# Kernel optimization log

Hardware: AMD Instinct MI355X
Metric: run time of the kernel (lower is better)

The kernel has to match this reference:

```python
import jax, jax.numpy as jnp
import numpy as np

EPS = 1e-5  # torch InstanceNorm1d default


def _instance_norm_lastdim(t):
    # torch InstanceNorm1d applied to (b*h, n, d): normalizes over last axis d
    # per (b, h, n) with biased variance, no affine.
    mu = jnp.mean(t, axis=-1, keepdims=True)
    var = jnp.var(t, axis=-1, keepdims=True)
    return (t - mu) * jax.lax.rsqrt(var + EPS)


def setup_inputs() -> dict:
    key = jax.random.key(0)
    k1, k2, k3, k4 = jax.random.split(key, 4)
    b, n, dim = 4, 8192, 128
    heads, dim_head = 8, 64
    inner = heads * dim_head
    x = jax.random.normal(k1, (b, n, dim), dtype=jnp.float32)
    # nn.Linear(dim, inner*3, bias=False): weight (out, in); we store transposed (in, out)
    w_qkv = jax.random.normal(k2, (dim, inner * 3), dtype=jnp.float32) * (1.0 / np.sqrt(dim))
    w_out = jax.random.normal(k3, (inner, dim), dtype=jnp.float32) * (1.0 / np.sqrt(inner))
    b_out = jax.random.normal(k4, (dim,), dtype=jnp.float32) * 0.01
    return {"x": x, "w_qkv": w_qkv, "w_out": w_out, "b_out": b_out}


def reference(x, w_qkv, w_out, b_out):
    b, n, _ = x.shape
    heads, dim_head = 8, 64
    qkv = x @ w_qkv  # (b, n, 3*inner)
    q, k, v = jnp.split(qkv, 3, axis=-1)

    def to_heads(t):
        return t.reshape(b, n, heads, dim_head).transpose(0, 2, 1, 3)  # b h n d

    q, k, v = to_heads(q), to_heads(k), to_heads(v)
    # galerkin: norm k and v (InstanceNorm over dim_head axis)
    k = _instance_norm_lastdim(k)
    v = _instance_norm_lastdim(v)
    dots = jnp.einsum('bhnd,bhne->bhde', k, v)      # K^T V, small (d x d)
    out = jnp.einsum('bhnd,bhde->bhne', q, dots) * (1.0 / n)
    out = out.transpose(0, 2, 1, 3).reshape(b, n, heads * dim_head)
    return out @ w_out + b_out
```

## Files before the change

kernel.cpp:

```cpp
#include <hip/hip_runtime.h>

#define NN 8192
#define DIM 128

typedef short short8 __attribute__((ext_vector_type(8)));
typedef float f32x4 __attribute__((ext_vector_type(4)));

__device__ __forceinline__ unsigned short f2bf(float f) {
  unsigned int u = __float_as_uint(f);
  u = (u + 0x7FFFu + ((u >> 16) & 1u)) >> 16;
  return (unsigned short)u;
}
__device__ __forceinline__ unsigned int cvtpk(float a, float b) {
  unsigned int r;
  asm("v_cvt_pk_bf16_f32 %0, %1, %2" : "=v"(r) : "v"(a), "v"(b));
  return r;
}
__device__ __forceinline__ void gll16(const void* gsrc, void* ldst) {
  __builtin_amdgcn_global_load_lds(
      (const __attribute__((address_space(1))) unsigned int*)gsrc,
      (__attribute__((address_space(3))) unsigned int*)ldst, 16, 0, 0);
}
#define BAR_LGKM()                                          \
  do {                                                      \
    asm volatile("s_waitcnt lgkmcnt(0)" ::: "memory");      \
    __builtin_amdgcn_sched_barrier(0);                      \
    __builtin_amdgcn_s_barrier();                           \
    __builtin_amdgcn_sched_barrier(0);                      \
  } while (0)
#define BAR_VM()                                            \
  do {                                                      \
    asm volatile("s_waitcnt vmcnt(0)" ::: "memory");        \
    __builtin_amdgcn_sched_barrier(0);                      \
    __builtin_amdgcn_s_barrier();                           \
    __builtin_amdgcn_sched_barrier(0);                      \
  } while (0)

__global__ __launch_bounds__(256) void prep_kernel(const float* __restrict__ x,
                                                   const float* __restrict__ wqkv,
                                                   unsigned char* __restrict__ ximg,
                                                   unsigned char* __restrict__ wimg,
                                                   float* __restrict__ dots) {
  __shared__ __align__(16) unsigned char wb[32768];
  const int t = threadIdx.x;
  const int bx = blockIdx.x;
  if (bx < 1024) {
#pragma unroll
    for (int rep = 0; rep < 2; ++rep) {
      const int idx = bx * 512 + rep * 256 + t;
      const int bt = idx >> 10;
      const int o = (idx & 1023) << 4;
      const int r = o >> 8;
      const int q0 = o & 255;
      const int c0 = (q0 ^ ((r & 7) << 4)) >> 1;
      const float* src = x + ((size_t)(bt >> 7) * NN + (size_t)(bt & 127) * 64 + r) * DIM + c0;
      const float4 v0 = *(const float4*)src;
      const float4 v1 = *(const float4*)(src + 4);
      uint4 u;
      u.x = cvtpk(v0.x, v0.y);
      u.y = cvtpk(v0.z, v0.w);
      u.z = cvtpk(v1.x, v1.y);
      u.w = cvtpk(v1.z, v1.w);
      *(uint4*)(ximg + (size_t)idx * 16) = u;
    }
  } else if (bx < 1032) {
    const int h = bx - 1024;
    const int k = t >> 1;
    const int chalf = t & 1;
    const float* wp = wqkv + (size_t)k * 1536 + (chalf ? (1024 + h * 64) : (512 + h * 64));
    const float4* wp4 = (const float4*)wp;
    const int c0 = chalf * 64;
    float4 wv[16];
    float sum = 0.f;
#pragma unroll
    for (int jj = 0; jj < 16; ++jj) {
      wv[jj] = wp4[jj];
      sum += wv[jj].x + wv[jj].y + wv[jj].z + wv[jj].w;
    }
    const float mean = sum * (1.f / 64.f);
#pragma unroll
    for (int jj = 0; jj < 16; ++jj) {
      const int c = c0 + jj * 4;
      const unsigned int cx0 = (unsigned int)((c + 0) & 7) << 4;
      const unsigned int cx1 = (unsigned int)((c + 1) & 7) << 4;
      const unsigned int cx2 = (unsigned int)((c + 2) & 7) << 4;
      const unsigned int cx3 = (unsigned int)((c + 3) & 7) << 4;
      *(unsigned short*)(wb + (c + 0) * 256 + (((unsigned)(2 * k)) ^ cx0)) = f2bf(wv[jj].x - mean);
      *(unsigned short*)(wb + (c + 1) * 256 + (((unsigned)(2 * k)) ^ cx1)) = f2bf(wv[jj].y - mean);
      *(unsigned short*)(wb + (c + 2) * 256 + (((unsigned)(2 * k)) ^ cx2)) = f2bf(wv[jj].z - mean);
      *(unsigned short*)(wb + (c + 3) * 256 + (((unsigned)(2 * k)) ^ cx3)) = f2bf(wv[jj].w - mean);
    }
    __syncthreads();
    const uint4* s4 = (const uint4*)(wb + t * 128);
    uint4* d4 = (uint4*)(wimg + (size_t)h * 32768 + t * 128);
#pragma unroll
    for (int i = 0; i < 8; ++i) d4[i] = s4[i];
  } else {
    const int zb = bx - 1032;
    float4* dz = (float4*)dots + (size_t)zb * 4096 + t;
    const float4 z = make_float4(0.f, 0.f, 0.f, 0.f);
#pragma unroll
    for (int i = 0; i < 16; ++i) dz[i * 256] = z;
  }
}

__global__ __launch_bounds__(256, 4) void kv_dots_v4(const unsigned char* __restrict__ ximg,
                                                     const unsigned char* __restrict__ wimg,
                                                     float* __restrict__ dots) {
  __shared__ __align__(16) unsigned char smem[40960];
  unsigned char* const WB = smem;
  unsigned char* const KT = smem + 32768;
  unsigned char* const VT = smem + 36864;

  const int t = threadIdx.x;
  const int bx = blockIdx.x;
  const int h = bx >> 7;
  const int p = bx & 127;
  const int b = p >> 5;
  const int chunk = p & 31;

  const int wave = t >> 6;
  const int lane = t & 63;
  const int lb = lane & 15;
  const int kg = lane >> 4;
  const int g = wave & 1;
  const int ch = wave >> 1;
  const unsigned int lxor = (unsigned int)(lb & 7) << 4;
  const unsigned int rxor = (unsigned int)(lb & 3) << 4;

  const unsigned char* wsrc = wimg + (size_t)h * 32768;
  const unsigned char* xsrc = ximg + (size_t)(b * 128 + chunk * 4) * 16384;

#pragma unroll
  for (int i = 0; i < 8; ++i)
    gll16(wsrc + (i * 4 + wave) * 1024 + lane * 16, WB + (i * 4 + wave) * 1024);

  const int rrow = 16 * g + lb;
  short8 xf[4];
#pragma unroll
  for (int ks = 0; ks < 4; ++ks)
    xf[ks] = *(const short8*)(xsrc + rrow * 256 + (((unsigned)(ks * 64 + kg * 16)) ^ lxor));

  f32x4 dacc[4];
#pragma unroll
  for (int et = 0; et < 4; ++et) dacc[et] = (f32x4)0.f;

  BAR_VM();

  unsigned char* const MYT = ch ? VT : KT;

  for (int tile = 0; tile < 8; ++tile) {
    short8 xn[4];
    if (tile < 7) {
      const unsigned char* tb = xsrc + (size_t)((tile + 1) >> 1) * 16384 + (size_t)((tile + 1) & 1) * 8192;
#pragma unroll
      for (int ks = 0; ks < 4; ++ks)
        xn[ks] = *(const short8*)(tb + rrow * 256 + (((unsigned)(ks * 64 + kg * 16)) ^ lxor));
    }

    f32x4 acc[4];
#pragma unroll
    for (int ct = 0; ct < 4; ++ct) acc[ct] = (f32x4)0.f;
#pragma unroll
    for (int ks = 0; ks < 4; ++ks) {
      const unsigned int koff = ((unsigned)(ks * 64 + kg * 16)) ^ lxor;
#pragma unroll
      for (int ct = 0; ct < 4; ++ct) {
        const short8 bf = *(const short8*)(WB + (ch * 64 + ct * 16 + lb) * 256 + koff);
        acc[ct] = __builtin_amdgcn_mfma_f32_16x16x32_bf16(xf[ks], bf, acc[ct], 0, 0, 0);
      }
    }

    float sc[4];
#pragma unroll
    for (int e = 0; e < 4; ++e) {
      float s = acc[0][e] * acc[0][e] + acc[1][e] * acc[1][e] +
                acc[2][e] * acc[2][e] + acc[3][e] * acc[3][e];
      s += __shfl_xor(s, 1);
      s += __shfl_xor(s, 2);
      s += __shfl_xor(s, 4);
      s += __shfl_xor(s, 8);
      sc[e] = rsqrtf(s * (1.f / 64.f) + 1e-5f);
    }

    {
      const unsigned int rb = ((unsigned)(g * 32 + kg * 8)) ^ rxor;
#pragma unroll
      for (int ct = 0; ct < 4; ++ct) {
        uint2 w2;
        w2.x = cvtpk(acc[ct][0] * sc[0], acc[ct][1] * sc[1]);
        w2.y = cvtpk(acc[ct][2] * sc[2], acc[ct][3] * sc[3]);
        *(uint2*)(MYT + (ct * 16 + lb) * 64 + rb) = w2;
      }
    }
    BAR_LGKM();

    {
      const unsigned int soff = ((unsigned)(kg * 16)) ^ rxor;
      const short8 a = *(const short8*)(KT + (wave * 16 + lb) * 64 + soff);
#pragma unroll
      for (int et = 0; et < 4; ++et) {
        const short8 bf = *(const short8*)(VT + (et * 16 + lb) * 64 + soff);
        dacc[et] = __builtin_amdgcn_mfma_f32_16x16x32_bf16(a, bf, dacc[et], 0, 0, 0);
      }
    }
    BAR_LGKM();

#pragma unroll
    for (int ks = 0; ks < 4; ++ks) xf[ks] = xn[ks];
  }

  float* dp = dots + (size_t)(b * 8 + h) * 4096;
#pragma unroll
  for (int et = 0; et < 4; ++et) {
#pragma unroll
    for (int reg = 0; reg < 4; ++reg) {
      const int d = wave * 16 + kg * 4 + reg;
      const int e = et * 16 + lb;
      atomicAdd(&dp[d * 64 + e], dacc[et][reg]);
    }
  }
}

template <int TR>
__global__ __launch_bounds__(256) void tw_kernel(const float* __restrict__ wqkv,
                                                 const float* __restrict__ wout,
                                                 const float* __restrict__ dots,
                                                 float* __restrict__ part) {
  __shared__ __align__(16) float ds[64 * 66];
  __shared__ __align__(16) float wqT[64 * 36];
  __shared__ __align__(16) float Ts[32 * 66];
  __shared__ __align__(16) float wos[64 * 132];

  const int blk = blockIdx.x;
  const int bh = blk >> 2;
  const int cq = blk & 3;
  const int h = bh & 7;
  const int t = threadIdx.x;

  for (int i = t; i < 4096; i += 256)
    ds[(i >> 6) * 66 + (i & 63)] = dots[(size_t)bh * 4096 + i];

  for (int i = t; i < 2048; i += 256) {
    const int d = i >> 5;
    const int c = i & 31;
    wqT[d * 36 + c] = wqkv[(size_t)(cq * 32 + c) * 1536 + h * 64 + d];
  }

  for (int i = t; i < 2048; i += 256) {
    const int e = i >> 5;
    const int jj = (i & 31) * 4;
    *(float4*)&wos[e * 132 + jj] = *(const float4*)(wout + (size_t)(h * 64 + e) * 128 + jj);
  }
  __syncthreads();

  {
    const int c = t >> 3;
    const int e0 = (t & 7) * 8;
    float acc[8];
#pragma unroll
    for (int q = 0; q < 8; ++q) acc[q] = 0.f;
    for (int d = 0; d < 64; ++d) {
      const float wq = wqT[d * 36 + c];
      const float4 d0 = *(const float4*)&ds[d * 66 + e0];
      const float4 d1 = *(const float4*)&ds[d * 66 + e0 + 4];
      acc[0] += wq * d0.x; acc[1] += wq * d0.y; acc[2] += wq * d0.z; acc[3] += wq * d0.w;
      acc[4] += wq * d1.x; acc[5] += wq * d1.y; acc[6] += wq * d1.z; acc[7] += wq * d1.w;
    }
    *(float4*)&Ts[c * 66 + e0] = make_float4(acc[0], acc[1], acc[2], acc[3]);
    *(float4*)&Ts[c * 66 + e0 + 4] = make_float4(acc[4], acc[5], acc[6], acc[7]);
  }
  __syncthreads();

  {
    const int c = t >> 3;
    const int j0 = (t & 7) * 16;
    float acc[16];
#pragma unroll
    for (int q = 0; q < 16; ++q) acc[q] = 0.f;
    for (int e = 0; e < 64; ++e) {
      const float tv = Ts[c * 66 + e];
#pragma unroll
      for (int q = 0; q < 16; q += 4) {
        const float4 wv = *(const float4*)&wos[e * 132 + j0 + q];
        acc[q + 0] += tv * wv.x;
        acc[q + 1] += tv * wv.y;
        acc[q + 2] += tv * wv.z;
        acc[q + 3] += tv * wv.w;
      }
    }
    if (TR) {
      float* pp = part + (size_t)bh * 16384;
      const int cc = cq * 32 + c;
#pragma unroll
      for (int q = 0; q < 16; ++q) pp[(j0 + q) * 128 + cc] = acc[q];
    } else {
      float* pp = part + (size_t)bh * 16384 + (size_t)(cq * 32 + c) * 128 + j0;
#pragma unroll
      for (int q = 0; q < 16; q += 4)
        *(float4*)&pp[q] = make_float4(acc[q], acc[q + 1], acc[q + 2], acc[q + 3]);
    }
  }
}

__global__ __launch_bounds__(256) void bigw_reduce_v2(const float* __restrict__ part,
                                                      unsigned char* __restrict__ bigwimg) {
  const int idx = blockIdx.x * 256 + threadIdx.x;
  const int b = idx >> 11;
  const int o = (idx & 2047) << 4;
  const int j = o >> 8;
  const int q0 = o & 255;
  const int c0 = (q0 ^ ((j & 7) << 4)) >> 1;
  float s[8];
#pragma unroll
  for (int i = 0; i < 8; ++i) s[i] = 0.f;
  const float* pb = part + (size_t)b * 8 * 16384 + j * 128 + c0;
#pragma unroll
  for (int hh = 0; hh < 8; ++hh) {
    const float4 p0 = *(const float4*)(pb + hh * 16384);
    const float4 p1 = *(const float4*)(pb + hh * 16384 + 4);
    s[0] += p0.x; s[1] += p0.y; s[2] += p0.z; s[3] += p0.w;
    s[4] += p1.x; s[5] += p1.y; s[6] += p1.z; s[7] += p1.w;
  }
  const float inv_n = 1.f / (float)NN;
  uint4 u;
  u.x = cvtpk(s[0] * inv_n, s[1] * inv_n);
  u.y = cvtpk(s[2] * inv_n, s[3] * inv_n);
  u.z = cvtpk(s[4] * inv_n, s[5] * inv_n);
  u.w = cvtpk(s[6] * inv_n, s[7] * inv_n);
  *(uint4*)(bigwimg + (size_t)idx * 16) = u;
}

__global__ __launch_bounds__(256) void out_v2(const unsigned char* __restrict__ ximg,
                                              const unsigned char* __restrict__ bigwimg,
                                              const float* __restrict__ bout,
                                              float* __restrict__ out) {
  __shared__ __align__(16) unsigned char smem[49152];
  unsigned char* const XB = smem;
  unsigned char* const WJ = smem + 16384;

  const int t = threadIdx.x;
  const int bx = blockIdx.x;
  const int b = bx >> 7;
  const int tile = bx & 127;

  const int wave = t >> 6;
  const int lane = t & 63;
  const int lb = lane & 15;
  const int kg = lane >> 4;
  const unsigned int lxor = (unsigned int)(lb & 7) << 4;

  const unsigned char* wsrc = bigwimg + (size_t)b * 32768;
  const unsigned char* xsrc = ximg + (size_t)(b * 128 + tile) * 16384;

#pragma unroll
  for (int i = 0; i < 8; ++i)
    gll16(wsrc + (wave * 8 + i) * 1024 + lane * 16, WJ + (wave * 8 + i) * 1024);
#pragma unroll
  for (int i = 0; i < 4; ++i)
    gll16(xsrc + (wave * 4 + i) * 1024 + lane * 16, XB + (wave * 4 + i) * 1024);

  float bias[8];
#pragma unroll
  for (int ct = 0; ct < 8; ++ct) bias[ct] = bout[ct * 16 + lb];

  BAR_VM();

  f32x4 acc[8];
#pragma unroll
  for (int ct = 0; ct < 8; ++ct) acc[ct] = (f32x4)0.f;
  const int arow = wave * 16 + lb;
#pragma unroll
  for (int ks = 0; ks < 4; ++ks) {
    const unsigned int koff = (unsigned int)(ks * 64 + kg * 16);
    const short8 a = *(const short8*)(XB + arow * 256 + (koff ^ lxor));
#pragma unroll
    for (int ct = 0; ct < 8; ++ct) {
      const short8 bf = *(const short8*)(WJ + (ct * 16 + lb) * 256 + (koff ^ lxor));
      acc[ct] = __builtin_amdgcn_mfma_f32_16x16x32_bf16(a, bf, acc[ct], 0, 0, 0);
    }
  }

  float* op = out + (size_t)(b * NN + tile * 64 + 16 * wave + kg * 4) * DIM;
#pragma unroll
  for (int ct = 0; ct < 8; ++ct) {
#pragma unroll
    for (int reg = 0; reg < 4; ++reg) {
      op[reg * DIM + ct * 16 + lb] = acc[ct][reg] + bias[ct];
    }
  }
}

__global__ __launch_bounds__(256) void zero_dots_fb(float* __restrict__ dots) {
  float4* dz = (float4*)dots + (size_t)blockIdx.x * 4096 + threadIdx.x;
  const float4 z = make_float4(0.f, 0.f, 0.f, 0.f);
#pragma unroll
  for (int i = 0; i < 16; ++i) dz[i * 256] = z;
}

__global__ __launch_bounds__(256) void kv_dots_fb(const float* __restrict__ x,
                                                  const float* __restrict__ wqkv,
                                                  float* __restrict__ dots) {
  __shared__ __align__(16) unsigned char smem[49152];
  unsigned char* const XB = smem;
  unsigned char* const KT = smem;
  unsigned char* const VT = smem + 8192;
  unsigned char* const WB = smem + 16384;

  const int t = threadIdx.x;
  const int bx = blockIdx.x;
  const int h = bx >> 7;
  const int p = bx & 127;
  const int b = p >> 5;
  const int chunk = p & 31;
  const int row0 = chunk * 256;

  const int wave = t >> 6;
  const int lane = t & 63;
  const int lb = lane & 15;
  const int kg = lane >> 4;
  const unsigned int lxor = (unsigned int)(lb & 7) << 4;

  {
    const int k = t >> 1;
    const int chalf = t & 1;
    const float* wp = wqkv + (size_t)k * 1536 + (chalf ? (1024 + h * 64) : (512 + h * 64));
    const float4* wp4 = (const float4*)wp;
    const int c0 = chalf * 64;
    float4 wv[16];
    float sum = 0.f;
#pragma unroll
    for (int jj = 0; jj < 16; ++jj) {
      wv[jj] = wp4[jj];
      sum += wv[jj].x + wv[jj].y + wv[jj].z + wv[jj].w;
    }
    const float mean = sum * (1.f / 64.f);
#pragma unroll
    for (int jj = 0; jj < 16; ++jj) {
      const int c = c0 + jj * 4;
      const unsigned int cx0 = (unsigned int)((c + 0) & 7) << 4;
      const unsigned int cx1 = (unsigned int)((c + 1) & 7) << 4;
      const unsigned int cx2 = (unsigned int)((c + 2) & 7) << 4;
      const unsigned int cx3 = (unsigned int)((c + 3) & 7) << 4;
      *(unsigned short*)(WB + (c + 0) * 256 + (((unsigned)(2 * k)) ^ cx0)) = f2bf(wv[jj].x - mean);
      *(unsigned short*)(WB + (c + 1) * 256 + (((unsigned)(2 * k)) ^ cx1)) = f2bf(wv[jj].y - mean);
      *(unsigned short*)(WB + (c + 2) * 256 + (((unsigned)(2 * k)) ^ cx2)) = f2bf(wv[jj].z - mean);
      *(unsigned short*)(WB + (c + 3) * 256 + (((unsigned)(2 * k)) ^ cx3)) = f2bf(wv[jj].w - mean);
    }
  }

  f32x4 dacc[4];
#pragma unroll
  for (int nt = 0; nt < 4; ++nt) dacc[nt] = (f32x4)0.f;

  __syncthreads();

  for (int tile = 0; tile < 4; ++tile) {
    const int rowbase = row0 + tile * 64;
    __syncthreads();
    {
      const int r = t >> 2;
      const int cb = (t & 3) * 32;
      const float4* gp4 = (const float4*)(x + (size_t)(b * NN + rowbase + r) * DIM + cb);
      const unsigned int rxor = (unsigned int)(r & 7) << 4;
#pragma unroll
      for (int jj = 0; jj < 4; ++jj) {
        const float4 v0 = gp4[2 * jj];
        const float4 v1 = gp4[2 * jj + 1];
        uint4 u;
        u.x = cvtpk(v0.x, v0.y);
        u.y = cvtpk(v0.z, v0.w);
        u.z = cvtpk(v1.x, v1.y);
        u.w = cvtpk(v1.z, v1.w);
        *(uint4*)(XB + r * 256 + (((unsigned)(2 * cb + 16 * jj)) ^ rxor)) = u;
      }
    }
    __syncthreads();

    f32x4 acc[8];
#pragma unroll
    for (int ct = 0; ct < 8; ++ct) acc[ct] = (f32x4)0.f;
    const int arow = wave * 16 + lb;
#pragma unroll
    for (int ks = 0; ks < 4; ++ks) {
      const unsigned int koff = (unsigned int)(ks * 64 + kg * 16);
      const short8 a = *(const short8*)(XB + arow * 256 + (koff ^ lxor));
#pragma unroll
      for (int ct = 0; ct < 8; ++ct) {
        const short8 bf = *(const short8*)(WB + (ct * 16 + lb) * 256 + (koff ^ lxor));
        acc[ct] = __builtin_amdgcn_mfma_f32_16x16x32_bf16(a, bf, acc[ct], 0, 0, 0);
      }
    }

    float kscale[4];
#pragma unroll
    for (int e = 0; e < 4; ++e) {
      float sk = acc[0][e] * acc[0][e] + acc[1][e] * acc[1][e] +
                 acc[2][e] * acc[2][e] + acc[3][e] * acc[3][e];
      float sv = acc[4][e] * acc[4][e] + acc[5][e] * acc[5][e] +
                 acc[6][e] * acc[6][e] + acc[7][e] * acc[7][e];
      sk += __shfl_xor(sk, 1); sv += __shfl_xor(sv, 1);
      sk += __shfl_xor(sk, 2); sv += __shfl_xor(sv, 2);
      sk += __shfl_xor(sk, 4); sv += __shfl_xor(sv, 4);
      sk += __shfl_xor(sk, 8); sv += __shfl_xor(sv, 8);
      kscale[e] = rsqrtf(sk * (1.f / 64.f) + 1e-5f) * rsqrtf(sv * (1.f / 64.f) + 1e-5f);
    }

    __syncthreads();
    {
      const unsigned int rb2 = (unsigned int)(32 * wave + kg * 8);
#pragma unroll
      for (int ct = 0; ct < 4; ++ct) {
        uint2 w;
        w.x = cvtpk(acc[ct][0] * kscale[0], acc[ct][1] * kscale[1]);
        w.y = cvtpk(acc[ct][2] * kscale[2], acc[ct][3] * kscale[3]);
        *(uint2*)(KT + (ct * 16 + lb) * 128 + (rb2 ^ lxor)) = w;
      }
#pragma unroll
      for (int ct = 4; ct < 8; ++ct) {
        uint2 w;
        w.x = cvtpk(acc[ct][0], acc[ct][1]);
        w.y = cvtpk(acc[ct][2], acc[ct][3]);
        *(uint2*)(VT + ((ct - 4) * 16 + lb) * 128 + (rb2 ^ lxor)) = w;
      }
    }
    __syncthreads();

#pragma unroll
    for (int ks2 = 0; ks2 < 2; ++ks2) {
      const unsigned int koff = (unsigned int)(ks2 * 64 + kg * 16);
      const short8 a = *(const short8*)(KT + (wave * 16 + lb) * 128 + (koff ^ lxor));
#pragma unroll
      for (int nt = 0; nt < 4; ++nt) {
        const short8 bf = *(const short8*)(VT + (nt * 16 + lb) * 128 + (koff ^ lxor));
        dacc[nt] = __builtin_amdgcn_mfma_f32_16x16x32_bf16(a, bf, dacc[nt], 0, 0, 0);
      }
    }
  }

  float* dp = dots + (size_t)(b * 8 + h) * 4096;
#pragma unroll
  for (int nt = 0; nt < 4; ++nt) {
#pragma unroll
    for (int reg = 0; reg < 4; ++reg) {
      const int d = 16 * wave + kg * 4 + reg;
      const int e = nt * 16 + lb;
      atomicAdd(&dp[d * 64 + e], dacc[nt][reg]);
    }
  }
}

__global__ __launch_bounds__(256) void bigw_reduce_fb(const float* __restrict__ part,
                                                      float* __restrict__ bigw) {
  const int i = blockIdx.x * 256 + threadIdx.x;
  const int b = i >> 14;
  const int cj = i & 16383;
  const float* pp = part + (size_t)b * 8 * 16384 + cj;
  float s = 0.f;
#pragma unroll
  for (int h = 0; h < 8; ++h) s += pp[h * 16384];
  bigw[i] = s * (1.f / (float)NN);
}

__global__ __launch_bounds__(256) void out_fb(const float* __restrict__ x,
                                              const float* __restrict__ bigw,
                                              const float* __restrict__ bout,
                                              float* __restrict__ out) {
  __shared__ __align__(16) unsigned char smem[49152];
  unsigned char* const XB = smem;
  unsigned char* const WB = smem + 16384;

  const int t = threadIdx.x;
  const int bx = blockIdx.x;
  const int b = bx >> 7;
  const int rowbase = (bx & 127) * 64;

  const int wave = t >> 6;
  const int lane = t & 63;
  const int lb = lane & 15;
  const int kg = lane >> 4;
  const unsigned int lxor = (unsigned int)(lb & 7) << 4;

  {
    const int c = t >> 1;
    const int jhalf = t & 1;
    const float4* wp4 = (const float4*)(bigw + (size_t)b * 16384 + (size_t)c * 128 + jhalf * 64);
    const int j0 = jhalf * 64;
#pragma unroll
    for (int q = 0; q < 16; ++q) {
      const float4 v = wp4[q];
      const int j = j0 + q * 4;
      const unsigned int jx0 = (unsigned int)((j + 0) & 7) << 4;
      const unsigned int jx1 = (unsigned int)((j + 1) & 7) << 4;
      const unsigned int jx2 = (unsigned int)((j + 2) & 7) << 4;
      const unsigned int jx3 = (unsigned int)((j + 3) & 7) << 4;
      *(unsigned short*)(WB + (j + 0) * 256 + (((unsigned)(2 * c)) ^ jx0)) = f2bf(v.x);
      *(unsigned short*)(WB + (j + 1) * 256 + (((unsigned)(2 * c)) ^ jx1)) = f2bf(v.y);
      *(unsigned short*)(WB + (j + 2) * 256 + (((unsigned)(2 * c)) ^ jx2)) = f2bf(v.z);
      *(unsigned short*)(WB + (j + 3) * 256 + (((unsigned)(2 * c)) ^ jx3)) = f2bf(v.w);
    }
  }

  float bias[8];
#pragma unroll
  for (int ct = 0; ct < 8; ++ct) bias[ct] = bout[ct * 16 + lb];

  {
    const int r = t >> 2;
    const int cb = (t & 3) * 32;
    const float4* gp4 = (const float4*)(x + (size_t)(b * NN + rowbase + r) * DIM + cb);
    const unsigned int rxor = (unsigned int)(r & 7) << 4;
#pragma unroll
    for (int jj = 0; jj < 4; ++jj) {
      const float4 v0 = gp4[2 * jj];
      const float4 v1 = gp4[2 * jj + 1];
      uint4 u;
      u.x = cvtpk(v0.x, v0.y);
      u.y = cvtpk(v0.z, v0.w);
      u.z = cvtpk(v1.x, v1.y);
      u.w = cvtpk(v1.z, v1.w);
      *(uint4*)(XB + r * 256 + (((unsigned)(2 * cb + 16 * jj)) ^ rxor)) = u;
    }
  }
  __syncthreads();

  f32x4 acc[8];
#pragma unroll
  for (int ct = 0; ct < 8; ++ct) acc[ct] = (f32x4)0.f;
  const int arow = wave * 16 + lb;
#pragma unroll
  for (int ks = 0; ks < 4; ++ks) {
    const unsigned int koff = (unsigned int)(ks * 64 + kg * 16);
    const short8 a = *(const short8*)(XB + arow * 256 + (koff ^ lxor));
#pragma unroll
    for (int ct = 0; ct < 8; ++ct) {
      const short8 bf = *(const short8*)(WB + (ct * 16 + lb) * 256 + (koff ^ lxor));
      acc[ct] = __builtin_amdgcn_mfma_f32_16x16x32_bf16(a, bf, acc[ct], 0, 0, 0);
    }
  }

  float* op = out + (size_t)(b * NN + rowbase + 16 * wave + kg * 4) * DIM;
#pragma unroll
  for (int ct = 0; ct < 8; ++ct) {
#pragma unroll
    for (int reg = 0; reg < 4; ++reg) {
      op[reg * DIM + ct * 16 + lb] = acc[ct][reg] + bias[ct];
    }
  }
}

extern "C" void kernel_launch(void* const* d_in, const int* in_sizes, int n_in,
                              void* d_out, int out_size, void* d_ws, size_t ws_size,
                              hipStream_t stream) {
  (void)in_sizes; (void)n_in; (void)out_size;
  const float* x = (const float*)d_in[0];
  const float* wqkv = (const float*)d_in[1];
  const float* wout = (const float*)d_in[2];
  const float* bout = (const float*)d_in[3];
  float* out = (float*)d_out;

  const size_t NEED = 8388608ull + 262144ull + 131072ull + 524288ull + 2097152ull;
  if (ws_size >= NEED) {
    unsigned char* ximg = (unsigned char*)d_ws;
    unsigned char* wimg = ximg + 8388608;
    unsigned char* bigwimg = wimg + 262144;
    float* dots = (float*)(bigwimg + 131072);
    float* part = dots + 131072;

    hipLaunchKernelGGL(prep_kernel, dim3(1040), dim3(256), 0, stream, x, wqkv, ximg, wimg, dots);
    hipLaunchKernelGGL(kv_dots_v4, dim3(1024), dim3(256), 0, stream, ximg, wimg, dots);
    hipLaunchKernelGGL((tw_kernel<1>), dim3(128), dim3(256), 0, stream, wqkv, wout, dots, part);
    hipLaunchKernelGGL(bigw_reduce_v2, dim3(32), dim3(256), 0, stream, part, bigwimg);
    hipLaunchKernelGGL(out_v2, dim3(512), dim3(256), 0, stream, ximg, bigwimg, bout, out);
  } else {
    float* dots = (float*)d_ws;
    float* part = dots + 131072;
    float* bigw = part + 524288;
    hipLaunchKernelGGL(zero_dots_fb, dim3(8), dim3(256), 0, stream, dots);
    hipLaunchKernelGGL(kv_dots_fb, dim3(1024), dim3(256), 0, stream, x, wqkv, dots);
    hipLaunchKernelGGL((tw_kernel<0>), dim3(128), dim3(256), 0, stream, wqkv, wout, dots, part);
    hipLaunchKernelGGL(bigw_reduce_fb, dim3(256), dim3(256), 0, stream, part, bigw);
    hipLaunchKernelGGL(out_fb, dim3(512), dim3(256), 0, stream, x, bigw, bout, out);
  }
}
```

Measured before the change: 65.87 us.

## Fuse bigw reduction into tw via atomics and double-buffer kv_dots LDS

```diff
diff --git a/kernel.cpp b/kernel.cpp
--- a/kernel.cpp
+++ b/kernel.cpp
@@ -35,12 +35,20 @@
     __builtin_amdgcn_s_barrier();                           \
     __builtin_amdgcn_sched_barrier(0);                      \
   } while (0)
+#define BAR_BOTH()                                                  \
+  do {                                                              \
+    asm volatile("s_waitcnt vmcnt(0) lgkmcnt(0)" ::: "memory");     \
+    __builtin_amdgcn_sched_barrier(0);                              \
+    __builtin_amdgcn_s_barrier();                                   \
+    __builtin_amdgcn_sched_barrier(0);                              \
+  } while (0)
 
 __global__ __launch_bounds__(256) void prep_kernel(const float* __restrict__ x,
                                                    const float* __restrict__ wqkv,
                                                    unsigned char* __restrict__ ximg,
                                                    unsigned char* __restrict__ wimg,
-                                                   float* __restrict__ dots) {
+                                                   float* __restrict__ dots,
+                                                   float* __restrict__ bigw) {
   __shared__ __align__(16) unsigned char wb[32768];
   const int t = threadIdx.x;
   const int bx = blockIdx.x;
@@ -95,22 +103,26 @@
     uint4* d4 = (uint4*)(wimg + (size_t)h * 32768 + t * 128);
 #pragma unroll
     for (int i = 0; i < 8; ++i) d4[i] = s4[i];
-  } else {
+  } else if (bx < 1040) {
     const int zb = bx - 1032;
     float4* dz = (float4*)dots + (size_t)zb * 4096 + t;
     const float4 z = make_float4(0.f, 0.f, 0.f, 0.f);
 #pragma unroll
     for (int i = 0; i < 16; ++i) dz[i * 256] = z;
-  }
-}
-
-__global__ __launch_bounds__(256, 4) void kv_dots_v4(const unsigned char* __restrict__ ximg,
+  } else {
+    const int zb = bx - 1040;
+    float4* bz = (float4*)bigw + (size_t)zb * 4096 + t;
+    const float4 z = make_float4(0.f, 0.f, 0.f, 0.f);
+#pragma unroll
+    for (int i = 0; i < 16; ++i) bz[i * 256] = z;
+  }
+}
+
+__global__ __launch_bounds__(256, 3) void kv_dots_v5(const unsigned char* __restrict__ ximg,
                                                      const unsigned char* __restrict__ wimg,
                                                      float* __restrict__ dots) {
-  __shared__ __align__(16) unsigned char smem[40960];
+  __shared__ __align__(16) unsigned char smem[49152];
   unsigned char* const WB = smem;
-  unsigned char* const KT = smem + 32768;
-  unsigned char* const VT = smem + 36864;
 
   const int t = threadIdx.x;
   const int bx = blockIdx.x;
@@ -147,8 +159,6 @@
 
   BAR_VM();
 
-  unsigned char* const MYT = ch ? VT : KT;
-
   for (int tile = 0; tile < 8; ++tile) {
     short8 xn[4];
     if (tile < 7) {
@@ -183,7 +193,9 @@
       sc[e] = rsqrtf(s * (1.f / 64.f) + 1e-5f);
     }
 
+    unsigned char* const BUF = smem + 32768 + (tile & 1) * 8192;
     {
+      unsigned char* const MYT = BUF + ch * 4096;
       const unsigned int rb = ((unsigned)(g * 32 + kg * 8)) ^ rxor;
 #pragma unroll
       for (int ct = 0; ct < 4; ++ct) {
@@ -197,14 +209,13 @@
 
     {
       const unsigned int soff = ((unsigned)(kg * 16)) ^ rxor;
-      const short8 a = *(const short8*)(KT + (wave * 16 + lb) * 64 + soff);
+      const short8 a = *(const short8*)(BUF + (wave * 16 + lb) * 64 + soff);
 #pragma unroll
       for (int et = 0; et < 4; ++et) {
-        const short8 bf = *(const short8*)(VT + (et * 16 + lb) * 64 + soff);
+        const short8 bf = *(const short8*)(BUF + 4096 + (et * 16 + lb) * 64 + soff);
         dacc[et] = __builtin_amdgcn_mfma_f32_16x16x32_bf16(a, bf, dacc[et], 0, 0, 0);
       }
     }
-    BAR_LGKM();
 
 #pragma unroll
     for (int ks = 0; ks < 4; ++ks) xf[ks] = xn[ks];
@@ -222,11 +233,10 @@
   }
 }
 
-template <int TR>
-__global__ __launch_bounds__(256) void tw_kernel(const float* __restrict__ wqkv,
-                                                 const float* __restrict__ wout,
-                                                 const float* __restrict__ dots,
-                                                 float* __restrict__ part) {
+__global__ __launch_bounds__(256) void tw_v3(const float* __restrict__ wqkv,
+                                             const float* __restrict__ wout,
+                                             const float* __restrict__ dots,
+                                             float* __restrict__ bigw) {
   __shared__ __align__(16) float ds[64 * 66];
   __shared__ __align__(16) float wqT[64 * 36];
   __shared__ __align__(16) float Ts[32 * 66];
@@ -289,50 +299,15 @@
         acc[q + 3] += tv * wv.w;
       }
     }
-    if (TR) {
-      float* pp = part + (size_t)bh * 16384;
-      const int cc = cq * 32 + c;
-#pragma unroll
-      for (int q = 0; q < 16; ++q) pp[(j0 + q) * 128 + cc] = acc[q];
-    } else {
-      float* pp = part + (size_t)bh * 16384 + (size_t)(cq * 32 + c) * 128 + j0;
-#pragma unroll
-      for (int q = 0; q < 16; q += 4)
-        *(float4*)&pp[q] = make_float4(acc[q], acc[q + 1], acc[q + 2], acc[q + 3]);
-    }
-  }
-}
-
-__global__ __launch_bounds__(256) void bigw_reduce_v2(const float* __restrict__ part,
-                                                      unsigned char* __restrict__ bigwimg) {
-  const int idx = blockIdx.x * 256 + threadIdx.x;
-  const int b = idx >> 11;
-  const int o = (idx & 2047) << 4;
-  const int j = o >> 8;
-  const int q0 = o & 255;
-  const int c0 = (q0 ^ ((j & 7) << 4)) >> 1;
-  float s[8];
-#pragma unroll
-  for (int i = 0; i < 8; ++i) s[i] = 0.f;
-  const float* pb = part + (size_t)b * 8 * 16384 + j * 128 + c0;
-#pragma unroll
-  for (int hh = 0; hh < 8; ++hh) {
-    const float4 p0 = *(const float4*)(pb + hh * 16384);
-    const float4 p1 = *(const float4*)(pb + hh * 16384 + 4);
-    s[0] += p0.x; s[1] += p0.y; s[2] += p0.z; s[3] += p0.w;
-    s[4] += p1.x; s[5] += p1.y; s[6] += p1.z; s[7] += p1.w;
-  }
-  const float inv_n = 1.f / (float)NN;
-  uint4 u;
-  u.x = cvtpk(s[0] * inv_n, s[1] * inv_n);
-  u.y = cvtpk(s[2] * inv_n, s[3] * inv_n);
-  u.z = cvtpk(s[4] * inv_n, s[5] * inv_n);
-  u.w = cvtpk(s[6] * inv_n, s[7] * inv_n);
-  *(uint4*)(bigwimg + (size_t)idx * 16) = u;
-}
-
-__global__ __launch_bounds__(256) void out_v2(const unsigned char* __restrict__ ximg,
-                                              const unsigned char* __restrict__ bigwimg,
+    const float inv_n = 1.f / (float)NN;
+    float* bp = bigw + (size_t)(bh >> 3) * 16384 + (size_t)(cq * 32 + c) * 128 + j0;
+#pragma unroll
+    for (int q = 0; q < 16; ++q) atomicAdd(&bp[q], acc[q] * inv_n);
+  }
+}
+
+__global__ __launch_bounds__(256) void out_v3(const unsigned char* __restrict__ ximg,
+                                              const float* __restrict__ bigw,
                                               const float* __restrict__ bout,
                                               float* __restrict__ out) {
   __shared__ __align__(16) unsigned char smem[49152];
@@ -350,21 +325,36 @@
   const int kg = lane >> 4;
   const unsigned int lxor = (unsigned int)(lb & 7) << 4;
 
-  const unsigned char* wsrc = bigwimg + (size_t)b * 32768;
   const unsigned char* xsrc = ximg + (size_t)(b * 128 + tile) * 16384;
-
-#pragma unroll
-  for (int i = 0; i < 8; ++i)
-    gll16(wsrc + (wave * 8 + i) * 1024 + lane * 16, WJ + (wave * 8 + i) * 1024);
 #pragma unroll
   for (int i = 0; i < 4; ++i)
     gll16(xsrc + (wave * 4 + i) * 1024 + lane * 16, XB + (wave * 4 + i) * 1024);
 
+  {
+    const int c = t >> 1;
+    const int jhalf = t & 1;
+    const float4* wp4 = (const float4*)(bigw + (size_t)b * 16384 + (size_t)c * 128 + jhalf * 64);
+    const int j0 = jhalf * 64;
+#pragma unroll
+    for (int q = 0; q < 16; ++q) {
+      const float4 v = wp4[q];
+      const int j = j0 + q * 4;
+      const unsigned int jx0 = (unsigned int)((j + 0) & 7) << 4;
+      const unsigned int jx1 = (unsigned int)((j + 1) & 7) << 4;
+      const unsigned int jx2 = (unsigned int)((j + 2) & 7) << 4;
+      const unsigned int jx3 = (unsigned int)((j + 3) & 7) << 4;
+      *(unsigned short*)(WJ + (j + 0) * 256 + (((unsigned)(2 * c)) ^ jx0)) = f2bf(v.x);
+      *(unsigned short*)(WJ + (j + 1) * 256 + (((unsigned)(2 * c)) ^ jx1)) = f2bf(v.y);
+      *(unsigned short*)(WJ + (j + 2) * 256 + (((unsigned)(2 * c)) ^ jx2)) = f2bf(v.z);
+      *(unsigned short*)(WJ + (j + 3) * 256 + (((unsigned)(2 * c)) ^ jx3)) = f2bf(v.w);
+    }
+  }
+
   float bias[8];
 #pragma unroll
   for (int ct = 0; ct < 8; ++ct) bias[ct] = bout[ct * 16 + lb];
 
-  BAR_VM();
+  BAR_BOTH();
 
   f32x4 acc[8];
 #pragma unroll
@@ -547,6 +537,79 @@
       const int e = nt * 16 + lb;
       atomicAdd(&dp[d * 64 + e], dacc[nt][reg]);
     }
+  }
+}
+
+__global__ __launch_bounds__(256) void tw_fb(const float* __restrict__ wqkv,
+                                             const float* __restrict__ wout,
+                                             const float* __restrict__ dots,
+                                             float* __restrict__ part) {
+  __shared__ __align__(16) float ds[64 * 66];
+  __shared__ __align__(16) float wqT[64 * 36];
+  __shared__ __align__(16) float Ts[32 * 66];
+  __shared__ __align__(16) float wos[64 * 132];
+
+  const int blk = blockIdx.x;
+  const int bh = blk >> 2;
+  const int cq = blk & 3;
+  const int h = bh & 7;
+  const int t = threadIdx.x;
+
+  for (int i = t; i < 4096; i += 256)
+    ds[(i >> 6) * 66 + (i & 63)] = dots[(size_t)bh * 4096 + i];
+
+  for (int i = t; i < 2048; i += 256) {
+    const int d = i >> 5;
+    const int c = i & 31;
+    wqT[d * 36 + c] = wqkv[(size_t)(cq * 32 + c) * 1536 + h * 64 + d];
+  }
+
+  for (int i = t; i < 2048; i += 256) {
+    const int e = i >> 5;
+    const int jj = (i & 31) * 4;
+    *(float4*)&wos[e * 132 + jj] = *(const float4*)(wout + (size_t)(h * 64 + e) * 128 + jj);
+  }
+  __syncthreads();
+
+  {
+    const int c = t >> 3;
+    const int e0 = (t & 7) * 8;
+    float acc[8];
+#pragma unroll
+    for (int q = 0; q < 8; ++q) acc[q] = 0.f;
+    for (int d = 0; d < 64; ++d) {
+      const float wq = wqT[d * 36 + c];
+      const float4 d0 = *(const float4*)&ds[d * 66 + e0];
+      const float4 d1 = *(const float4*)&ds[d * 66 + e0 + 4];
+      acc[0] += wq * d0.x; acc[1] += wq * d0.y; acc[2] += wq * d0.z; acc[3] += wq * d0.w;
+      acc[4] += wq * d1.x; acc[5] += wq * d1.y; acc[6] += wq * d1.z; acc[7] += wq * d1.w;
+    }
+    *(float4*)&Ts[c * 66 + e0] = make_float4(acc[0], acc[1], acc[2], acc[3]);
+    *(float4*)&Ts[c * 66 + e0 + 4] = make_float4(acc[4], acc[5], acc[6], acc[7]);
+  }
+  __syncthreads();
+
+  {
+    const int c = t >> 3;
+    const int j0 = (t & 7) * 16;
+    float acc[16];
+#pragma unroll
+    for (int q = 0; q < 16; ++q) acc[q] = 0.f;
+    for (int e = 0; e < 64; ++e) {
+      const float tv = Ts[c * 66 + e];
+#pragma unroll
+      for (int q = 0; q < 16; q += 4) {
+        const float4 wv = *(const float4*)&wos[e * 132 + j0 + q];
+        acc[q + 0] += tv * wv.x;
+        acc[q + 1] += tv * wv.y;
+        acc[q + 2] += tv * wv.z;
+        acc[q + 3] += tv * wv.w;
+      }
+    }
+    float* pp = part + (size_t)bh * 16384 + (size_t)(cq * 32 + c) * 128 + j0;
+#pragma unroll
+    for (int q = 0; q < 16; q += 4)
+      *(float4*)&pp[q] = make_float4(acc[q], acc[q + 1], acc[q + 2], acc[q + 3]);
   }
 }
 
@@ -659,26 +722,24 @@
   const float* bout = (const float*)d_in[3];
   float* out = (float*)d_out;
 
-  const size_t NEED = 8388608ull + 262144ull + 131072ull + 524288ull + 2097152ull;
+  const size_t NEED = 8388608ull + 262144ull + 524288ull + 262144ull;
   if (ws_size >= NEED) {
     unsigned char* ximg = (unsigned char*)d_ws;
     unsigned char* wimg = ximg + 8388608;
-    unsigned char* bigwimg = wimg + 262144;
-    float* dots = (float*)(bigwimg + 131072);
-    float* part = dots + 131072;
-
-    hipLaunchKernelGGL(prep_kernel, dim3(1040), dim3(256), 0, stream, x, wqkv, ximg, wimg, dots);
-    hipLaunchKernelGGL(kv_dots_v4, dim3(1024), dim3(256), 0, stream, ximg, wimg, dots);
-    hipLaunchKernelGGL((tw_kernel<1>), dim3(128), dim3(256), 0, stream, wqkv, wout, dots, part);
-    hipLaunchKernelGGL(bigw_reduce_v2, dim3(32), dim3(256), 0, stream, part, bigwimg);
-    hipLaunchKernelGGL(out_v2, dim3(512), dim3(256), 0, stream, ximg, bigwimg, bout, out);
+    float* dots = (float*)(wimg + 262144);
+    float* bigw = dots + 131072;
+
+    hipLaunchKernelGGL(prep_kernel, dim3(1044), dim3(256), 0, stream, x, wqkv, ximg, wimg, dots, bigw);
+    hipLaunchKernelGGL(kv_dots_v5, dim3(1024), dim3(256), 0, stream, ximg, wimg, dots);
+    hipLaunchKernelGGL(tw_v3, dim3(128), dim3(256), 0, stream, wqkv, wout, dots, bigw);
+    hipLaunchKernelGGL(out_v3, dim3(512), dim3(256), 0, stream, ximg, bigw, bout, out);
   } else {
     float* dots = (float*)d_ws;
     float* part = dots + 131072;
     float* bigw = part + 524288;
     hipLaunchKernelGGL(zero_dots_fb, dim3(8), dim3(256), 0, stream, dots);
     hipLaunchKernelGGL(kv_dots_fb, dim3(1024), dim3(256), 0, stream, x, wqkv, dots);
-    hipLaunchKernelGGL((tw_kernel<0>), dim3(128), dim3(256), 0, stream, wqkv, wout, dots, part);
+    hipLaunchKernelGGL(tw_fb, dim3(128), dim3(256), 0, stream, wqkv, wout, dots, part);
     hipLaunchKernelGGL(bigw_reduce_fb, dim3(256), dim3(256), 0, stream, part, bigw);
     hipLaunchKernelGGL(out_fb, dim3(512), dim3(256), 0, stream, x, bigw, bout, out);
   }
```

Measured after the change: 93.34 us. 1.42x slower.

## Replace atomic dots accumulation with per-block partials reduced in tw_kernel

Applied to the files above, without the earlier changes.

```diff
diff --git a/kernel.cpp b/kernel.cpp
--- a/kernel.cpp
+++ b/kernel.cpp
@@ -39,8 +39,7 @@
 __global__ __launch_bounds__(256) void prep_kernel(const float* __restrict__ x,
                                                    const float* __restrict__ wqkv,
                                                    unsigned char* __restrict__ ximg,
-                                                   unsigned char* __restrict__ wimg,
-                                                   float* __restrict__ dots) {
+                                                   unsigned char* __restrict__ wimg) {
   __shared__ __align__(16) unsigned char wb[32768];
   const int t = threadIdx.x;
   const int bx = blockIdx.x;
@@ -63,7 +62,7 @@
       u.w = cvtpk(v1.z, v1.w);
       *(uint4*)(ximg + (size_t)idx * 16) = u;
     }
-  } else if (bx < 1032) {
+  } else {
     const int h = bx - 1024;
     const int k = t >> 1;
     const int chalf = t & 1;
@@ -95,18 +94,12 @@
     uint4* d4 = (uint4*)(wimg + (size_t)h * 32768 + t * 128);
 #pragma unroll
     for (int i = 0; i < 8; ++i) d4[i] = s4[i];
-  } else {
-    const int zb = bx - 1032;
-    float4* dz = (float4*)dots + (size_t)zb * 4096 + t;
-    const float4 z = make_float4(0.f, 0.f, 0.f, 0.f);
-#pragma unroll
-    for (int i = 0; i < 16; ++i) dz[i * 256] = z;
-  }
-}
-
-__global__ __launch_bounds__(256, 4) void kv_dots_v4(const unsigned char* __restrict__ ximg,
+  }
+}
+
+__global__ __launch_bounds__(256, 4) void kv_dots_v7(const unsigned char* __restrict__ ximg,
                                                      const unsigned char* __restrict__ wimg,
-                                                     float* __restrict__ dots) {
+                                                     float* __restrict__ dotspart) {
   __shared__ __align__(16) unsigned char smem[40960];
   unsigned char* const WB = smem;
   unsigned char* const KT = smem + 32768;
@@ -210,14 +203,14 @@
     for (int ks = 0; ks < 4; ++ks) xf[ks] = xn[ks];
   }
 
-  float* dp = dots + (size_t)(b * 8 + h) * 4096;
+  float* dp = dotspart + (size_t)bx * 4096;
 #pragma unroll
   for (int et = 0; et < 4; ++et) {
 #pragma unroll
     for (int reg = 0; reg < 4; ++reg) {
       const int d = wave * 16 + kg * 4 + reg;
       const int e = et * 16 + lb;
-      atomicAdd(&dp[d * 64 + e], dacc[et][reg]);
+      dp[d * 64 + e] = dacc[et][reg];
     }
   }
 }
@@ -238,8 +231,18 @@
   const int h = bh & 7;
   const int t = threadIdx.x;
 
-  for (int i = t; i < 4096; i += 256)
-    ds[(i >> 6) * 66 + (i & 63)] = dots[(size_t)bh * 4096 + i];
+  if (TR) {
+    const float* pb = dots + (size_t)(h * 128 + (bh >> 3) * 32) * 4096;
+    for (int i = t; i < 4096; i += 256) {
+      float s = 0.f;
+#pragma unroll 8
+      for (int c = 0; c < 32; ++c) s += pb[(size_t)c * 4096 + i];
+      ds[(i >> 6) * 66 + (i & 63)] = s;
+    }
+  } else {
+    for (int i = t; i < 4096; i += 256)
+      ds[(i >> 6) * 66 + (i & 63)] = dots[(size_t)bh * 4096 + i];
+  }
 
   for (int i = t; i < 2048; i += 256) {
     const int d = i >> 5;
@@ -659,17 +662,17 @@
   const float* bout = (const float*)d_in[3];
   float* out = (float*)d_out;
 
-  const size_t NEED = 8388608ull + 262144ull + 131072ull + 524288ull + 2097152ull;
+  const size_t NEED = 8388608ull + 262144ull + 131072ull + 16777216ull + 2097152ull;
   if (ws_size >= NEED) {
     unsigned char* ximg = (unsigned char*)d_ws;
     unsigned char* wimg = ximg + 8388608;
     unsigned char* bigwimg = wimg + 262144;
-    float* dots = (float*)(bigwimg + 131072);
-    float* part = dots + 131072;
-
-    hipLaunchKernelGGL(prep_kernel, dim3(1040), dim3(256), 0, stream, x, wqkv, ximg, wimg, dots);
-    hipLaunchKernelGGL(kv_dots_v4, dim3(1024), dim3(256), 0, stream, ximg, wimg, dots);
-    hipLaunchKernelGGL((tw_kernel<1>), dim3(128), dim3(256), 0, stream, wqkv, wout, dots, part);
+    float* dotspart = (float*)(bigwimg + 131072);
+    float* part = dotspart + 4194304;
+
+    hipLaunchKernelGGL(prep_kernel, dim3(1032), dim3(256), 0, stream, x, wqkv, ximg, wimg);
+    hipLaunchKernelGGL(kv_dots_v7, dim3(1024), dim3(256), 0, stream, ximg, wimg, dotspart);
+    hipLaunchKernelGGL((tw_kernel<1>), dim3(128), dim3(256), 0, stream, wqkv, wout, dotspart, part);
     hipLaunchKernelGGL(bigw_reduce_v2, dim3(32), dim3(256), 0, stream, part, bigwimg);
     hipLaunchKernelGGL(out_v2, dim3(512), dim3(256), 0, stream, ximg, bigwimg, bout, out);
   } else {
```

After: 83.68 us. 27.0% more time.
